# Performance work log

Hardware: AMD Instinct MI355X
Metric: run time of the kernel (lower is better)

Reference implementation:

```python
import jax, jax.numpy as jnp
import numpy as np

N = 50000   # nodes
E = 300000  # directed edges
IN = 512
H = 256
OUT = 256
K = 4096    # K_target; since K < N, pooled node count Kc == K statically


def setup_inputs() -> dict:
    key = jax.random.key(0)
    ks = jax.random.split(key, 8)
    x = jax.random.normal(ks[0], (N, IN), jnp.float32)
    edge_index = jax.random.randint(ks[1], (2, E), 0, N)
    W1 = jax.random.normal(ks[2], (IN, H), jnp.float32) / np.float32(np.sqrt(IN))
    b1 = jnp.zeros((H,), jnp.float32)
    W2 = jax.random.normal(ks[3], (H, OUT), jnp.float32) / np.float32(np.sqrt(H))
    b2 = jnp.zeros((OUT,), jnp.float32)
    w_score = jax.random.normal(ks[4], (H,), jnp.float32) / np.float32(np.sqrt(H))
    W_skip = jax.random.normal(ks[5], (H, OUT), jnp.float32) / np.float32(np.sqrt(H))
    b_skip = jnp.zeros((OUT,), jnp.float32)
    return dict(x=x, edge_index=edge_index, W1=W1, b1=b1, W2=W2, b2=b2,
                w_score=w_score, W_skip=W_skip, b_skip=b_skip)


def _gcn_sparse(x, src, dst, W, b, n):
    # PyG GCNConv(add_self_loops=True, normalize=True): out = D^{-1/2}(A+I)D^{-1/2} x W + b,
    # degrees computed on dst after adding self loops.
    h = x @ W
    loop = jnp.arange(n)
    s = jnp.concatenate([src, loop])
    d = jnp.concatenate([dst, loop])
    deg = jax.ops.segment_sum(jnp.ones_like(d, h.dtype), d, num_segments=n)
    dinv = jnp.where(deg > 0, jax.lax.rsqrt(deg), 0.0)
    coef = (dinv[s] * dinv[d])[:, None]
    return jax.ops.segment_sum(h[s] * coef, d, num_segments=n) + b


def _forward(x, edge_index, W1, b1, W2, b2, w_score, W_skip, b_skip):
    n = x.shape[0]
    src, dst = edge_index[0], edge_index[1]

    # conv1 + relu (dropout is identity in eval mode)
    x1 = jax.nn.relu(_gcn_sparse(x, src, dst, W1, b1, n))
    raw = x1 @ w_score                       # [N] score (Linear, no bias)
    x1g = x1 * jnp.tanh(raw)[:, None]        # gated features

    # top-K node selection
    _, kept = jax.lax.top_k(raw, K)          # sorted descending, like torch.topk
    keep_mask = jnp.zeros((n,), bool).at[kept].set(True)
    deg = jax.ops.segment_sum(jnp.ones((src.shape[0],), jnp.int32), src, num_segments=n)

    # cluster ids: kept nodes get 0..K-1 in topk order
    cid = jnp.full((n,), -1, jnp.int32).at[kept].set(jnp.arange(K, dtype=jnp.int32))

    # non-kept nodes join the kept (undirected) neighbor with max degree;
    # encode (degree, -node_id) so segment_max picks max degree, tie-break smallest id
    s_all = jnp.concatenate([src, dst])
    t_all = jnp.concatenate([dst, src])
    cand = jnp.where(keep_mask[t_all], deg[t_all] * n + (n - 1 - t_all), -1)
    best = jax.ops.segment_max(cand, s_all, num_segments=n)  # empty segs -> int min
    has = best >= 0
    best_t = (n - 1) - jnp.where(has, best % n, 0)
    # global fallback: kept node with max degree (tie-break: earliest in topk order)
    enc_k = deg[kept] * K + (K - 1 - jnp.arange(K))
    bg = kept[jnp.argmax(enc_k)]
    cid = jnp.where(keep_mask, cid, jnp.where(has, cid[best_t], cid[bg]))

    # mean pooling per cluster (pool_by_partition)
    sums = jax.ops.segment_sum(x1g, cid, num_segments=K)
    cnt = jnp.maximum(jax.ops.segment_sum(jnp.ones((n,), x.dtype), cid, num_segments=K), 1.0)
    xp = sums / cnt[:, None]

    # pooled edges with dedup + self-pair removal, as dense KxK adjacency (rows = dst)
    cu, cv = cid[src], cid[dst]
    A = jnp.zeros((K, K), x.dtype).at[cv, cu].max((cu != cv).astype(x.dtype))
    Ahat = A + jnp.eye(K, dtype=x.dtype)
    di = jax.lax.rsqrt(Ahat.sum(axis=1))     # deg >= 1 from self loops
    An = di[:, None] * Ahat * di[None, :]

    # conv2 on pooled graph, broadcast back, skip connection
    xp2 = An @ (xp @ W2) + b2
    return xp2[cid] + x1 @ W_skip + b_skip


def reference(x, edge_index, W1, b1, W2, b2, w_score, W_skip, b_skip):
    return _forward(x, edge_index, W1, b1, W2, b2, w_score, W_skip, b_skip)
```

## Files before the change

### kernel.cpp

```cpp
#include <hip/hip_runtime.h>
#include <hip/hip_bf16.h>

#define N_NODES 50000
#define E_EDGES 300000
#define IN_F 512
#define H_F 256
#define OUT_F 256
#define K_CL 4096
#define KW (K_CL / 32)
#define PCH 128
#define THRESH 192
#define MAXH 1024
#define NSPL 32
#define NB2 ((N_NODES + 255) / 256)
#define KBW ((N_NODES + 63) / 64 + 8)

typedef short bh8 __attribute__((ext_vector_type(8)));
typedef float f4 __attribute__((ext_vector_type(4)));
typedef unsigned short u16;
typedef unsigned long long u64;

__device__ __forceinline__ unsigned fkey(float f) {
    unsigned u = __float_as_uint(f);
    return (u & 0x80000000u) ? ~u : (u | 0x80000000u);
}

__device__ __forceinline__ u16 f2bf(float f) {
    __hip_bfloat16 b = __float2bfloat16(f);
    return *reinterpret_cast<u16*>(&b);
}

__device__ __forceinline__ float bf2f(u16 u) {
    return __uint_as_float(((unsigned)u) << 16);
}

__device__ __forceinline__ int getbit(const u64* __restrict__ bits, int i) {
    return (int)((bits[i >> 6] >> (i & 63)) & 1ULL);
}

__global__ __launch_bounds__(256) void init_nodes(int* cntD, int* degS,
                                                  unsigned long long* best_enc,
                                                  int* bgnode, int* heavycnt,
                                                  unsigned long long* bestpack) {
    int i = blockIdx.x * blockDim.x + threadIdx.x;
    if (i < N_NODES) { cntD[i] = 0; degS[i] = 0; best_enc[i] = 0ULL; }
    if (i == 0) { *heavycnt = 0; *bgnode = 0x7FFFFFFF; *bestpack = 0ULL; }
}

__global__ __launch_bounds__(256) void deg_edges(const int* __restrict__ src,
                                                 const int* __restrict__ dst,
                                                 int* cntD, int* degS) {
    int e = blockIdx.x * blockDim.x + threadIdx.x;
    if (e >= E_EDGES) return;
    atomicAdd(&cntD[dst[e]], 1);
    atomicAdd(&degS[src[e]], 1);
}

#define SBM 64
#define SBN 128
#define SBK 16
__global__ __launch_bounds__(256) void gemm_f32s(const float* __restrict__ A,
                                                 const float* __restrict__ B,
                                                 float* __restrict__ C,
                                                 int M, int Nc, int Kd) {
    __shared__ float As[2][SBM][SBK];
    __shared__ float Bs[2][SBK][SBN];
    int tid = threadIdx.x;
    int tx = tid & 15;
    int ty = tid >> 4;
    int lane = tid & 63;
    int wave = tid >> 6;
    int row0 = blockIdx.y * SBM, col0 = blockIdx.x * SBN;
    float acc[4][8] = {};

    int arow = wave * 16 + (lane >> 2);
    int acolf = ((((lane & 3) * 16) ^ (((lane >> 4) & 1) << 5)) >> 2);

    auto stage_B = [&](int k0, int bb) {
        #pragma unroll
        for (int u = 0; u < 2; ++u) {
            int chunk = wave * 2 + u;
            int krow = chunk * 2 + (lane >> 5);
            const float* gsrc = &B[(long)(k0 + krow) * Nc + col0 + (lane & 31) * 4];
            __builtin_amdgcn_global_load_lds(
                (const __attribute__((address_space(1))) void*)gsrc,
                (__attribute__((address_space(3))) void*)&Bs[bb][chunk * 2][0],
                16, 0, 0);
        }
    };
    auto stage_A = [&](int k0, int bb) {
        int gr = row0 + arow;
        if (gr > M - 1) gr = M - 1;
        const float* gsrc = &A[(long)gr * Kd + k0 + acolf];
        __builtin_amdgcn_global_load_lds(
            (const __attribute__((address_space(1))) void*)gsrc,
            (__attribute__((address_space(3))) void*)&As[bb][wave * 16][0],
            16, 0, 0);
    };
    auto compute = [&](int bb) {
        #pragma unroll
        for (int kq = 0; kq < 4; ++kq) {
            float4 af[4];
            #pragma unroll
            for (int i = 0; i < 4; ++i) {
                int row = ty * 4 + i;
                int cb = ((kq * 16 ^ (((row >> 2) & 1) << 5)) >> 2);
                af[i] = *(const float4*)&As[bb][row][cb];
            }
            #pragma unroll
            for (int kk = 0; kk < 4; ++kk) {
                int k = kq * 4 + kk;
                float4 b0 = *(const float4*)&Bs[bb][k][tx * 4];
                float4 b1 = *(const float4*)&Bs[bb][k][tx * 4 + 64];
                float bv[8] = {b0.x, b0.y, b0.z, b0.w, b1.x, b1.y, b1.z, b1.w};
                float av[4] = {af[0][kk], af[1][kk], af[2][kk], af[3][kk]};
                #pragma unroll
                for (int i = 0; i < 4; ++i)
                    #pragma unroll
                    for (int j = 0; j < 8; ++j)
                        acc[i][j] += av[i] * bv[j];
            }
        }
    };

    stage_B(0, 0);
    stage_A(0, 0);
    __syncthreads();
    int nt = Kd / SBK;
    for (int t = 0; t < nt; ++t) {
        int cb = t & 1;
        if (t + 1 < nt) {
            stage_B(SBK * (t + 1), cb ^ 1);
            stage_A(SBK * (t + 1), cb ^ 1);
        }
        compute(cb);
        __syncthreads();
    }

    #pragma unroll
    for (int i = 0; i < 4; ++i) {
        int gr = row0 + ty * 4 + i;
        if (gr >= M) continue;
        float4 o0 = {acc[i][0], acc[i][1], acc[i][2], acc[i][3]};
        float4 o1 = {acc[i][4], acc[i][5], acc[i][6], acc[i][7]};
        *(float4*)&C[(long)gr * Nc + col0 + tx * 4] = o0;
        *(float4*)&C[(long)gr * Nc + col0 + 64 + tx * 4] = o1;
    }
}

__global__ __launch_bounds__(256) void pack_W2(const float* __restrict__ Wa, u16* Bpa,
                                               const float* __restrict__ Wb, u16* Bpb) {
    int k = blockIdx.x & 255;
    const float* W = (blockIdx.x < 256) ? Wa : Wb;
    u16* Bp = (blockIdx.x < 256) ? Bpa : Bpb;
    int col = threadIdx.x;
    int kb = k >> 5, g = (k >> 3) & 3, j = k & 7;
    Bp[(((long)(kb * 4 + g) * 256) + col) * 8 + j] = f2bf(W[(long)k * 256 + col]);
}

__global__ __launch_bounds__(256) void gemm_mfma(const u16* __restrict__ Ab,
                                                 const float* __restrict__ Af32,
                                                 const int* __restrict__ cnt,
                                                 const u16* __restrict__ Bp,
                                                 float* __restrict__ C,
                                                 int M,
                                                 const int* __restrict__ cid,
                                                 const float* __restrict__ xp2,
                                                 const float* __restrict__ bskip) {
    int tid = threadIdx.x;
    int w = tid >> 6, l = tid & 63;
    int lo16 = l & 15, hi4 = l >> 4;
    int arow = blockIdx.x * 64 + w * 16 + lo16;
    f4 acc[16];
    #pragma unroll
    for (int n = 0; n < 16; ++n) acc[n] = (f4){0.f, 0.f, 0.f, 0.f};

    float s = 1.f;
    if (Af32 && arow < M) s = 1.f / fmaxf((float)cnt[arow], 1.f);

    #pragma unroll
    for (int kb = 0; kb < 8; ++kb) {
        bh8 a = {0, 0, 0, 0, 0, 0, 0, 0};
        if (arow < M) {
            if (Af32) {
                float4 v0 = *(const float4*)&Af32[(long)arow * 256 + kb * 32 + hi4 * 8];
                float4 v1 = *(const float4*)&Af32[(long)arow * 256 + kb * 32 + hi4 * 8 + 4];
                u16 tmp[8] = {f2bf(v0.x * s), f2bf(v0.y * s), f2bf(v0.z * s), f2bf(v0.w * s),
                              f2bf(v1.x * s), f2bf(v1.y * s), f2bf(v1.z * s), f2bf(v1.w * s)};
                a = *(const bh8*)tmp;
            } else {
                a = *(const bh8*)&Ab[(long)arow * 256 + kb * 32 + hi4 * 8];
            }
        }
        const u16* bbase = &Bp[(((long)(kb * 4 + hi4)) * 256 + lo16) * 8];
        #pragma unroll
        for (int n = 0; n < 16; ++n) {
            bh8 b = *(const bh8*)&bbase[(long)n * 128];
            acc[n] = __builtin_amdgcn_mfma_f32_16x16x32_bf16(a, b, acc[n], 0, 0, 0);
        }
    }

    int orow0 = blockIdx.x * 64 + w * 16 + hi4 * 4;
    #pragma unroll
    for (int r = 0; r < 4; ++r) {
        int gr = orow0 + r;
        if (gr >= M) continue;
        long rb = (long)gr * 256;
        const float* xrow = cid ? (xp2 + (long)cid[gr] * 256) : nullptr;
        #pragma unroll
        for (int n = 0; n < 16; ++n) {
            int gc = n * 16 + lo16;
            float v = acc[n][r];
            if (cid) v += xrow[gc] + bskip[gc];
            C[rb + gc] = v;
        }
    }
}

__global__ __launch_bounds__(256) void scan_l1(const int* __restrict__ cnt,
                                               int* bsum, int n, float* dinv) {
    __shared__ int s[256];
    int t = threadIdx.x;
    int i = blockIdx.x * 256 + t;
    int v = (i < n) ? cnt[i] : 0;
    if (dinv && i < n) dinv[i] = rsqrtf((float)v + 1.0f);
    s[t] = v;
    __syncthreads();
    for (int off = 128; off > 0; off >>= 1) {
        if (t < off) s[t] += s[t + off];
        __syncthreads();
    }
    if (t == 0) bsum[blockIdx.x] = s[0];
}

__global__ __launch_bounds__(256) void scan_l2(const int* __restrict__ bsum,
                                               int* bstart, int nb) {
    __shared__ int s[256];
    int t = threadIdx.x;
    int v = (t < nb) ? bsum[t] : 0;
    s[t] = v;
    __syncthreads();
    for (int off = 1; off < 256; off <<= 1) {
        int a = (t >= off) ? s[t - off] : 0;
        __syncthreads();
        s[t] += a;
        __syncthreads();
    }
    if (t < nb) bstart[t] = s[t] - v;
}

__global__ __launch_bounds__(256) void scan_l3(const int* __restrict__ cnt,
                                               const int* __restrict__ bstart,
                                               int* start, int* cur, int n) {
    __shared__ int s[256];
    int t = threadIdx.x;
    int i = blockIdx.x * 256 + t;
    int v = (i < n) ? cnt[i] : 0;
    s[t] = v;
    __syncthreads();
    for (int off = 1; off < 256; off <<= 1) {
        int a = (t >= off) ? s[t - off] : 0;
        __syncthreads();
        s[t] += a;
        __syncthreads();
    }
    int st = bstart[blockIdx.x] + s[t] - v;
    if (i < n) { start[i] = st; cur[i] = st; }
    if (i == n - 1) start[n] = st + v;
}

__global__ __launch_bounds__(256) void csr_scatter(const int* __restrict__ src,
                                                   const int* __restrict__ dst,
                                                   int* cur, int* csr) {
    int e = blockIdx.x * blockDim.x + threadIdx.x;
    if (e >= E_EDGES) return;
    int d = dst[e];
    int p = atomicAdd(&cur[d], 1);
    csr[p] = src[e];
}

__global__ __launch_bounds__(64) void agg_fused(const float* __restrict__ h,
                                                const float* __restrict__ dinv,
                                                const int* __restrict__ rowptr,
                                                const int* __restrict__ csr,
                                                const float* __restrict__ b1,
                                                const float* __restrict__ w_score,
                                                u16* __restrict__ x1b,
                                                float* __restrict__ raw) {
    int i = blockIdx.x;
    int l = threadIdx.x;
    float di_ = dinv[i];
    long hb = (long)i * H_F;
    float sc = di_ * di_;
    float a0 = sc * h[hb + l];
    float a1 = sc * h[hb + l + 64];
    float a2 = sc * h[hb + l + 128];
    float a3 = sc * h[hb + l + 192];
    int p0 = rowptr[i], p1 = rowptr[i + 1];
    for (int t = p0; t < p1; ++t) {
        int s = csr[t];
        float cf = dinv[s] * di_;
        long sb = (long)s * H_F;
        a0 += cf * h[sb + l];
        a1 += cf * h[sb + l + 64];
        a2 += cf * h[sb + l + 128];
        a3 += cf * h[sb + l + 192];
    }
    float v0 = fmaxf(a0 + b1[l], 0.f);
    float v1 = fmaxf(a1 + b1[l + 64], 0.f);
    float v2 = fmaxf(a2 + b1[l + 128], 0.f);
    float v3 = fmaxf(a3 + b1[l + 192], 0.f);
    x1b[hb + l] = f2bf(v0);
    x1b[hb + l + 64] = f2bf(v1);
    x1b[hb + l + 128] = f2bf(v2);
    x1b[hb + l + 192] = f2bf(v3);
    float r0 = v0 * w_score[l];
    float r1 = v1 * w_score[l + 64];
    float r2 = v2 * w_score[l + 128];
    float r3 = v3 * w_score[l + 192];
    float t1 = r0 + r2;
    float t2 = r1 + r3;
    float s2 = t1 + t2;
    #pragma unroll
    for (int off = 32; off > 0; off >>= 1)
        s2 += __shfl_xor(s2, off, 64);
    if (l == 0) raw[i] = s2;
}

__global__ __launch_bounds__(1024) void topk_select(const float* __restrict__ raw,
                                                    unsigned* outT, int* outNeedEq) {
    __shared__ unsigned hist[256];
    __shared__ unsigned sh_prefix;
    __shared__ int sh_k;
    int tid = threadIdx.x;
    if (tid == 0) { sh_prefix = 0; sh_k = K_CL; }
    __syncthreads();
    for (int byte = 3; byte >= 0; --byte) {
        if (tid < 256) hist[tid] = 0;
        __syncthreads();
        unsigned prefix = sh_prefix;
        unsigned known_mask = (byte == 3) ? 0u : (0xFFFFFFFFu << ((byte + 1) * 8));
        for (int i = tid; i < N_NODES; i += 1024) {
            unsigned key = fkey(raw[i]);
            if ((key & known_mask) == prefix)
                atomicAdd(&hist[(key >> (byte * 8)) & 255], 1u);
        }
        __syncthreads();
        if (tid == 0) {
            int kk = sh_k;
            int cum = 0;
            int v = 255;
            for (; v > 0; --v) {
                int c = (int)hist[v];
                if (cum + c >= kk) break;
                cum += c;
            }
            sh_prefix = prefix | ((unsigned)v << (byte * 8));
            sh_k = kk - cum;
        }
        __syncthreads();
    }
    if (tid == 0) { *outT = sh_prefix; *outNeedEq = sh_k; }
}

__global__ __launch_bounds__(256) void topk_count(const float* __restrict__ raw,
                                                  const unsigned* pT,
                                                  int* bGt, int* bEq) {
    __shared__ int sg[256], se[256];
    unsigned T = *pT;
    int t = threadIdx.x;
    int i = blockIdx.x * 256 + t;
    int gt = 0, eq = 0;
    if (i < N_NODES) {
        unsigned k = fkey(raw[i]);
        gt = k > T; eq = (k == T);
    }
    sg[t] = gt; se[t] = eq;
    __syncthreads();
    for (int off = 128; off > 0; off >>= 1) {
        if (t < off) { sg[t] += sg[t + off]; se[t] += se[t + off]; }
        __syncthreads();
    }
    if (t == 0) { bGt[blockIdx.x] = sg[0]; bEq[blockIdx.x] = se[0]; }
}

__global__ __launch_bounds__(256) void scan_blocks(const int* __restrict__ bGt,
                                                   const int* __restrict__ bEq,
                                                   int* gtStart, int* eqStart) {
    __shared__ int sg[256], se[256];
    int t = threadIdx.x;
    int vg = (t < NB2) ? bGt[t] : 0;
    int ve = (t < NB2) ? bEq[t] : 0;
    sg[t] = vg; se[t] = ve;
    __syncthreads();
    for (int off = 1; off < 256; off <<= 1) {
        int a = (t >= off) ? sg[t - off] : 0;
        int b = (t >= off) ? se[t - off] : 0;
        __syncthreads();
        sg[t] += a; se[t] += b;
        __syncthreads();
    }
    if (t < NB2) { gtStart[t] = sg[t] - vg; eqStart[t] = se[t] - ve; }
    if (t == 255) gtStart[NB2] = sg[255];
}

__global__ __launch_bounds__(256) void topk_assign(const float* __restrict__ raw,
                                                   const unsigned* pT, const int* pNeedEq,
                                                   const int* __restrict__ degS,
                                                   const int* __restrict__ gtStart,
                                                   const int* __restrict__ eqStart,
                                                   u64* keep_bits, int* cid,
                                                   unsigned long long* bestpack) {
    __shared__ int sg[256], se[256];
    unsigned T = *pT;
    int needEq = *pNeedEq;
    int totalGt = gtStart[NB2];
    int b = blockIdx.x, t = threadIdx.x;
    int i = b * 256 + t;
    int gt = 0, eq = 0;
    unsigned k = 0;
    if (i < N_NODES) {
        k = fkey(raw[i]);
        gt = k > T; eq = (k == T);
    }
    sg[t] = gt; se[t] = eq;
    __syncthreads();
    for (int off = 1; off < 256; off <<= 1) {
        int a = (t >= off) ? sg[t - off] : 0;
        int c = (t >= off) ? se[t - off] : 0;
        __syncthreads();
        sg[t] += a; se[t] += c;
        __syncthreads();
    }
    int eg = sg[t] - gt, ee = se[t] - eq;
    int kp = 0;
    unsigned long long p = 0ULL;
    if (i < N_NODES) {
        int c = -1;
        if (gt) { kp = 1; c = gtStart[b] + eg; }
        else if (eq) {
            int r = eqStart[b] + ee;
            if (r < needEq) { kp = 1; c = totalGt + r; }
        }
        cid[i] = c;
        if (kp) p = ((unsigned long long)(unsigned)degS[i] << 32) | k;
    }
    u64 ball = __ballot(kp);
    if ((t & 63) == 0) keep_bits[(b * 256 + t) >> 6] = ball;
    #pragma unroll
    for (int o = 32; o > 0; o >>= 1) {
        unsigned long long q = __shfl_xor((long long)p, o, 64);
        if (q > p) p = q;
    }
    if ((t & 63) == 0 && p) atomicMax(bestpack, p);
}

__global__ __launch_bounds__(256) void bg_node(const u64* __restrict__ keep_bits,
                                               const int* __restrict__ degS,
                                               const float* __restrict__ raw,
                                               const unsigned long long* bestpack, int* bgnode) {
    int i = blockIdx.x * blockDim.x + threadIdx.x;
    if (i < N_NODES && getbit(keep_bits, i)) {
        unsigned long long p = ((unsigned long long)(unsigned)degS[i] << 32) | fkey(raw[i]);
        if (p == *bestpack) atomicMin(bgnode, i);
    }
}

__global__ __launch_bounds__(256) void neigh_edges(const int* __restrict__ src,
                                                   const int* __restrict__ dst,
                                                   const u64* __restrict__ keep_bits,
                                                   const int* __restrict__ degS,
                                                   unsigned long long* best_enc) {
    int e = blockIdx.x * blockDim.x + threadIdx.x;
    if (e >= 2 * E_EDGES) return;
    int s, t;
    if (e < E_EDGES) { s = src[e]; t = dst[e]; }
    else { s = dst[e - E_EDGES]; t = src[e - E_EDGES]; }
    if (!getbit(keep_bits, s) && getbit(keep_bits, t)) {
        unsigned long long enc =
            (unsigned long long)((long long)degS[t] * N_NODES + (N_NODES - 1 - t)) + 1ULL;
        atomicMax(&best_enc[s], enc);
    }
}

__global__ __launch_bounds__(256) void resolve_cid(const u64* __restrict__ keep_bits,
                                                   const unsigned long long* __restrict__ best_enc,
                                                   const int* __restrict__ bgnode, int* cid) {
    int i = blockIdx.x * blockDim.x + threadIdx.x;
    if (i >= N_NODES) return;
    if (getbit(keep_bits, i)) return;
    unsigned long long v = best_enc[i];
    if (v > 0ULL) {
        long long enc = (long long)(v - 1ULL);
        int t = (N_NODES - 1) - (int)(enc % N_NODES);
        cid[i] = cid[t];
    } else {
        cid[i] = cid[*bgnode];
    }
}

#define NPB 1024
__global__ __launch_bounds__(256) void ccount2(const int* __restrict__ cid, int* ccnt) {
    __shared__ int hist[K_CL];
    for (int t = threadIdx.x; t < K_CL; t += 256) hist[t] = 0;
    __syncthreads();
    int base = blockIdx.x * NPB;
    #pragma unroll
    for (int u = 0; u < NPB / 256; ++u) {
        int idx = base + u * 256 + threadIdx.x;
        if (idx < N_NODES) atomicAdd(&hist[cid[idx]], 1);
    }
    __syncthreads();
    for (int t = threadIdx.x; t < K_CL; t += 256) {
        int hh = hist[t];
        if (hh) atomicAdd(&ccnt[t], hh);
    }
}

__global__ __launch_bounds__(256) void cscatter2(const int* __restrict__ cid,
                                                 int* ccur, int* clist) {
    __shared__ int hist[K_CL];
    for (int t = threadIdx.x; t < K_CL; t += 256) hist[t] = 0;
    __syncthreads();
    int base = blockIdx.x * NPB;
    int myc[NPB / 256], myr[NPB / 256];
    #pragma unroll
    for (int u = 0; u < NPB / 256; ++u) {
        int idx = base + u * 256 + threadIdx.x;
        if (idx < N_NODES) { myc[u] = cid[idx]; myr[u] = atomicAdd(&hist[myc[u]], 1); }
        else myc[u] = -1;
    }
    __syncthreads();
    for (int t = threadIdx.x; t < K_CL; t += 256) {
        int hh = hist[t];
        if (hh) hist[t] = atomicAdd(&ccur[t], hh);
    }
    __syncthreads();
    #pragma unroll
    for (int u = 0; u < NPB / 256; ++u)
        if (myc[u] >= 0) clist[hist[myc[u]] + myr[u]] = base + u * 256 + threadIdx.x;
}

__global__ __launch_bounds__(256) void pool_chunk(const u16* __restrict__ x1b,
                                                  const float* __restrict__ raw,
                                                  const int* __restrict__ clist,
                                                  const int* __restrict__ cid,
                                                  float* xp) {
    __shared__ int s_node[PCH];
    __shared__ int s_c[PCH];
    __shared__ float s_g[PCH];
    int j = threadIdx.x;
    int base = blockIdx.x * PCH;
    int m = N_NODES - base; if (m > PCH) m = PCH;
    for (int t = j; t < m; t += 256) {
        int nd = clist[base + t];
        s_node[t] = nd;
        s_c[t] = cid[nd];
        s_g[t] = tanhf(raw[nd]);
    }
    __syncthreads();
    float acc = 0.f;
    int cprev = s_c[0];
    for (int t = 0; t < m; t += 4) {
        int mm = m - t; if (mm > 4) mm = 4;
        float v[4];
        #pragma unroll
        for (int u = 0; u < 4; ++u)
            if (u < mm) v[u] = bf2f(x1b[(long)s_node[t + u] * H_F + j]);
        #pragma unroll
        for (int u = 0; u < 4; ++u) {
            if (u < mm) {
                int c = s_c[t + u];
                if (c != cprev) {
                    atomicAdd(&xp[(long)cprev * H_F + j], acc);
                    acc = 0.f;
                    cprev = c;
                }
                acc += s_g[t + u] * v[u];
            }
        }
    }
    atomicAdd(&xp[(long)cprev * H_F + j], acc);
}

__global__ __launch_bounds__(256) void build_Abits(const int* __restrict__ src,
                                                   const int* __restrict__ dst,
                                                   const int* __restrict__ cid,
                                                   unsigned* Abits) {
    int e = blockIdx.x * blockDim.x + threadIdx.x;
    if (e >= E_EDGES) return;
    int cu = cid[src[e]], cv = cid[dst[e]];
    if (cu != cv) atomicOr(&Abits[(long)cv * KW + (cu >> 5)], 1u << (cu & 31));
}

__global__ __launch_bounds__(256) void pop_di2(const unsigned* __restrict__ Abits, float* di,
                                               int* nnzA, int* heavy, int* heavycnt) {
    int i = blockIdx.x * blockDim.x + threadIdx.x;
    if (i >= K_CL) return;
    int c = 0;
    for (int w = 0; w < KW; ++w) c += __popc(Abits[(long)i * KW + w]);
    di[i] = rsqrtf((float)c + 1.0f);
    nnzA[i] = c;
    if (c > THRESH) {
        int p = atomicAdd(heavycnt, 1);
        if (p < MAXH) heavy[p] = i;
    }
}

__global__ __launch_bounds__(256) void spmm_light(const unsigned* __restrict__ Abits,
                                                  const float* __restrict__ xpW2,
                                                  const float* __restrict__ di,
                                                  const float* __restrict__ b2,
                                                  const int* __restrict__ nnzA,
                                                  float* xp2) {
    __shared__ unsigned s_row[KW];
    __shared__ float s_part[3][256];
    int cv = blockIdx.x;
    if (nnzA[cv] > THRESH) return;
    int tid = threadIdx.x;
    int w = tid >> 6, l = tid & 63;
    if (tid < KW) s_row[tid] = Abits[(long)cv * KW + tid];
    __syncthreads();
    float4 a0 = {0.f, 0.f, 0.f, 0.f}, a1 = {0.f, 0.f, 0.f, 0.f};
    const float4* Y4 = (const float4*)xpW2;
    for (int wi = w * 32; wi < w * 32 + 32; wi += 2) {
        unsigned w0 = s_row[wi], w1 = s_row[wi + 1];
        while (w0 | w1) {
            if (w0) {
                int b = __ffs(w0) - 1; w0 &= w0 - 1;
                int cu = wi * 32 + b;
                float d = di[cu];
                float4 y = Y4[(long)cu * 64 + l];
                a0.x += d * y.x; a0.y += d * y.y; a0.z += d * y.z; a0.w += d * y.w;
            }
            if (w1) {
                int b = __ffs(w1) - 1; w1 &= w1 - 1;
                int cu = (wi + 1) * 32 + b;
                float d = di[cu];
                float4 y = Y4[(long)cu * 64 + l];
                a1.x += d * y.x; a1.y += d * y.y; a1.z += d * y.z; a1.w += d * y.w;
            }
        }
    }
    float4 acc = {a0.x + a1.x, a0.y + a1.y, a0.z + a1.z, a0.w + a1.w};
    if (w > 0) *(float4*)&s_part[w - 1][l * 4] = acc;
    __syncthreads();
    if (w == 0) {
        #pragma unroll
        for (int ww = 0; ww < 3; ++ww) {
            float4 p = *(float4*)&s_part[ww][l * 4];
            acc.x += p.x; acc.y += p.y; acc.z += p.z; acc.w += p.w;
        }
        float dv = di[cv];
        float4 ys = Y4[(long)cv * 64 + l];
        float4 o;
        o.x = dv * (acc.x + dv * ys.x) + b2[l * 4 + 0];
        o.y = dv * (acc.y + dv * ys.y) + b2[l * 4 + 1];
        o.z = dv * (acc.z + dv * ys.z) + b2[l * 4 + 2];
        o.w = dv * (acc.w + dv * ys.w) + b2[l * 4 + 3];
        *(float4*)&xp2[(long)cv * H_F + l * 4] = o;
    }
}

__global__ __launch_bounds__(256) void spmm_heavy(const unsigned* __restrict__ Abits,
                                                  const float* __restrict__ xpW2,
                                                  const float* __restrict__ di,
                                                  const int* __restrict__ heavy,
                                                  const int* __restrict__ heavycnt,
                                                  float* Zacc) {
    __shared__ float s_part[3][256];
    int hi = blockIdx.x;
    int cnt = *heavycnt; if (cnt > MAXH) cnt = MAXH;
    if (hi >= cnt) return;
    int cv = heavy[hi];
    int sp = blockIdx.y;
    int tid = threadIdx.x;
    int w = tid >> 6, l = tid & 63;
    int wi = sp * (KW / NSPL) + w;
    unsigned word = Abits[(long)cv * KW + wi];
    float4 acc = {0.f, 0.f, 0.f, 0.f};
    const float4* Y4 = (const float4*)xpW2;
    while (word) {
        int b = __ffs(word) - 1; word &= word - 1;
        int cu = wi * 32 + b;
        float d = di[cu];
        float4 y = Y4[(long)cu * 64 + l];
        acc.x += d * y.x; acc.y += d * y.y; acc.z += d * y.z; acc.w += d * y.w;
    }
    if (w > 0) *(float4*)&s_part[w - 1][l * 4] = acc;
    __syncthreads();
    if (w == 0) {
        #pragma unroll
        for (int ww = 0; ww < 3; ++ww) {
            float4 p = *(float4*)&s_part[ww][l * 4];
            acc.x += p.x; acc.y += p.y; acc.z += p.z; acc.w += p.w;
        }
        float* zp = &Zacc[(long)cv * H_F + l * 4];
        atomicAdd(zp + 0, acc.x);
        atomicAdd(zp + 1, acc.y);
        atomicAdd(zp + 2, acc.z);
        atomicAdd(zp + 3, acc.w);
    }
}

__global__ __launch_bounds__(256) void heavy_epi(const float* __restrict__ Zacc,
                                                 const float* __restrict__ xpW2,
                                                 const float* __restrict__ di,
                                                 const float* __restrict__ b2,
                                                 const int* __restrict__ heavy,
                                                 const int* __restrict__ heavycnt,
                                                 float* xp2) {
    int hi = blockIdx.x;
    int cnt = *heavycnt; if (cnt > MAXH) cnt = MAXH;
    if (hi >= cnt) return;
    int cv = heavy[hi];
    int j = threadIdx.x;
    float dv = di[cv];
    xp2[(long)cv * H_F + j] =
        dv * (Zacc[(long)cv * H_F + j] + dv * xpW2[(long)cv * H_F + j]) + b2[j];
}

static inline size_t align256(size_t x) { return (x + 255) & ~(size_t)255; }

extern "C" void kernel_launch(void* const* d_in, const int* in_sizes, int n_in,
                              void* d_out, int out_size, void* d_ws, size_t ws_size,
                              hipStream_t stream) {
    const float* x      = (const float*)d_in[0];
    const int*   eidx   = (const int*)d_in[1];
    const float* W1     = (const float*)d_in[2];
    const float* b1     = (const float*)d_in[3];
    const float* W2     = (const float*)d_in[4];
    const float* b2     = (const float*)d_in[5];
    const float* wscore = (const float*)d_in[6];
    const float* Wskip  = (const float*)d_in[7];
    const float* bskip  = (const float*)d_in[8];
    float* out = (float*)d_out;

    const int* src = eidx;
    const int* dst = eidx + E_EDGES;

    char* ws = (char*)d_ws;
    size_t off = 0;
    auto alloc = [&](size_t bytes) { char* p = ws + off; off += align256(bytes); return p; };

    float* h     = (float*)alloc((size_t)N_NODES * H_F * 4);
    u16*   x1b   = (u16*)alloc((size_t)N_NODES * H_F * 2);
    float* raw   = (float*)alloc((size_t)N_NODES * 4);
    float* dinv  = (float*)alloc((size_t)N_NODES * 4);
    int*   cntD  = (int*)alloc((size_t)N_NODES * 4);
    int*   degS  = (int*)alloc((size_t)N_NODES * 4);
    u64*   keep_bits = (u64*)alloc((size_t)KBW * 8);
    int*   cid   = (int*)alloc((size_t)N_NODES * 4);
    unsigned long long* best_enc = (unsigned long long*)alloc((size_t)N_NODES * 8);
    int*   rowptr= (int*)alloc((size_t)(N_NODES + 1) * 4);
    int*   cur   = (int*)alloc((size_t)N_NODES * 4);
    int*   csr   = (int*)alloc((size_t)E_EDGES * 4);
    int*   ccnt  = (int*)alloc((size_t)K_CL * 4);
    int*   cstart= (int*)alloc((size_t)(K_CL + 1) * 4);
    int*   ccur  = (int*)alloc((size_t)K_CL * 4);
    int*   clist = (int*)alloc((size_t)N_NODES * 4);
    int*   bGt   = (int*)alloc((size_t)NB2 * 4);
    int*   bEq   = (int*)alloc((size_t)NB2 * 4);
    int*   gtStart = (int*)alloc((size_t)(NB2 + 1) * 4);
    int*   eqStart = (int*)alloc((size_t)NB2 * 4);
    int*   bsum  = (int*)alloc((size_t)256 * 4);
    int*   bstart= (int*)alloc((size_t)256 * 4);
    char*  small = alloc(64);
    unsigned* selT = (unsigned*)(small + 0);
    int* needEq    = (int*)(small + 4);
    int* bgnode    = (int*)(small + 8);
    int* heavycnt  = (int*)(small + 12);
    unsigned long long* bestpack = (unsigned long long*)(small + 16);
    float* xp    = (float*)alloc((size_t)K_CL * H_F * 4);
    unsigned* Abits = (unsigned*)alloc((size_t)K_CL * KW * 4);
    float* Zacc  = (float*)alloc((size_t)K_CL * H_F * 4);
    float* di    = (float*)alloc((size_t)K_CL * 4);
    int*   nnzA  = (int*)alloc((size_t)K_CL * 4);
    int*   heavy = (int*)alloc((size_t)MAXH * 4);
    float* xpW2  = (float*)alloc((size_t)K_CL * H_F * 4);
    float* xp2   = (float*)alloc((size_t)K_CL * H_F * 4);
    u16*  BpS   = (u16*)alloc((size_t)H_F * OUT_F * 2);
    u16*  Bp2   = (u16*)alloc((size_t)H_F * H_F * 2);
    (void)ws_size; (void)n_in; (void)in_sizes; (void)out_size;

    int nb = NB2;
    int eb = (E_EDGES + 255) / 256;

    init_nodes<<<nb, 256, 0, stream>>>(cntD, degS, best_enc, bgnode, heavycnt, bestpack);
    deg_edges<<<eb, 256, 0, stream>>>(src, dst, cntD, degS);

    pack_W2<<<512, 256, 0, stream>>>(Wskip, BpS, W2, Bp2);

    {
        dim3 grid(H_F / SBN, (N_NODES + SBM - 1) / SBM);
        gemm_f32s<<<grid, 256, 0, stream>>>(x, W1, h, N_NODES, H_F, IN_F);
    }

    scan_l1<<<NB2, 256, 0, stream>>>(cntD, bsum, N_NODES, dinv);
    scan_l2<<<1, 256, 0, stream>>>(bsum, bstart, NB2);
    scan_l3<<<NB2, 256, 0, stream>>>(cntD, bstart, rowptr, cur, N_NODES);
    csr_scatter<<<eb, 256, 0, stream>>>(src, dst, cur, csr);
    agg_fused<<<N_NODES, 64, 0, stream>>>(h, dinv, rowptr, csr, b1, wscore, x1b, raw);

    topk_select<<<1, 1024, 0, stream>>>(raw, selT, needEq);
    topk_count<<<NB2, 256, 0, stream>>>(raw, selT, bGt, bEq);
    scan_blocks<<<1, 256, 0, stream>>>(bGt, bEq, gtStart, eqStart);
    topk_assign<<<NB2, 256, 0, stream>>>(raw, selT, needEq, degS, gtStart, eqStart,
                                         keep_bits, cid, bestpack);
    bg_node<<<nb, 256, 0, stream>>>(keep_bits, degS, raw, bestpack, bgnode);

    neigh_edges<<<(2 * E_EDGES + 255) / 256, 256, 0, stream>>>(src, dst, keep_bits, degS,
                                                               best_enc);
    resolve_cid<<<nb, 256, 0, stream>>>(keep_bits, best_enc, bgnode, cid);

    hipMemsetAsync(xp, 0, (size_t)K_CL * H_F * 4 * 2 + (size_t)K_CL * KW * 4, stream);

    hipMemsetAsync(ccnt, 0, (size_t)K_CL * 4, stream);
    {
        int cb = (N_NODES + NPB - 1) / NPB;
        ccount2<<<cb, 256, 0, stream>>>(cid, ccnt);
        scan_l1<<<K_CL / 256, 256, 0, stream>>>(ccnt, bsum, K_CL, nullptr);
        scan_l2<<<1, 256, 0, stream>>>(bsum, bstart, K_CL / 256);
        scan_l3<<<K_CL / 256, 256, 0, stream>>>(ccnt, bstart, cstart, ccur, K_CL);
        cscatter2<<<cb, 256, 0, stream>>>(cid, ccur, clist);
    }
    pool_chunk<<<(N_NODES + PCH - 1) / PCH, 256, 0, stream>>>(x1b, raw, clist, cid, xp);

    gemm_mfma<<<K_CL / 64, 256, 0, stream>>>(nullptr, xp, ccnt, Bp2, xpW2, K_CL,
                                             nullptr, nullptr, nullptr);

    build_Abits<<<eb, 256, 0, stream>>>(src, dst, cid, Abits);
    pop_di2<<<(K_CL + 255) / 256, 256, 0, stream>>>(Abits, di, nnzA, heavy, heavycnt);
    spmm_light<<<K_CL, 256, 0, stream>>>(Abits, xpW2, di, b2, nnzA, xp2);
    {
        dim3 hgrid(MAXH, NSPL);
        spmm_heavy<<<hgrid, 256, 0, stream>>>(Abits, xpW2, di, heavy, heavycnt, Zacc);
    }
    heavy_epi<<<MAXH, 256, 0, stream>>>(Zacc, xpW2, di, b2, heavy, heavycnt, xp2);

    gemm_mfma<<<(N_NODES + 63) / 64, 256, 0, stream>>>(x1b, nullptr, nullptr, BpS, out,
                                                       N_NODES, cid, xp2, bskip);
}
```

Measured before the change: 680.6 us.

## Parallelize top-k radix select across many blocks with per-byte histogram kernels

Replaces the single-block 1024-thread radix select over 50000 scores with four rounds of a grid-wide histogram kernel followed by a one-thread pick kernel. The prefix and remaining count now live in global memory and are initialized in init_nodes, and the per-byte histograms are zeroed by a memset. The goal is to remove the serial single-CU pass over all nodes. The cost is eight extra small kernel launches plus global atomics.

Result: faster. 659.5 us (-3.1%).

```diff
diff --git a/kernel.cpp b/kernel.cpp
--- a/kernel.cpp
+++ b/kernel.cpp
@@ -41,10 +41,14 @@
 __global__ __launch_bounds__(256) void init_nodes(int* cntD, int* degS,
                                                   unsigned long long* best_enc,
                                                   int* bgnode, int* heavycnt,
-                                                  unsigned long long* bestpack) {
+                                                  unsigned long long* bestpack,
+                                                  unsigned* selT, int* curk) {
     int i = blockIdx.x * blockDim.x + threadIdx.x;
     if (i < N_NODES) { cntD[i] = 0; degS[i] = 0; best_enc[i] = 0ULL; }
-    if (i == 0) { *heavycnt = 0; *bgnode = 0x7FFFFFFF; *bestpack = 0ULL; }
+    if (i == 0) {
+        *heavycnt = 0; *bgnode = 0x7FFFFFFF; *bestpack = 0ULL;
+        *selT = 0u; *curk = K_CL;
+    }
 }
 
 __global__ __launch_bounds__(256) void deg_edges(const int* __restrict__ src,
@@ -327,40 +331,38 @@
     if (l == 0) raw[i] = s2;
 }
 
-__global__ __launch_bounds__(1024) void topk_select(const float* __restrict__ raw,
-                                                    unsigned* outT, int* outNeedEq) {
-    __shared__ unsigned hist[256];
-    __shared__ unsigned sh_prefix;
-    __shared__ int sh_k;
-    int tid = threadIdx.x;
-    if (tid == 0) { sh_prefix = 0; sh_k = K_CL; }
-    __syncthreads();
-    for (int byte = 3; byte >= 0; --byte) {
-        if (tid < 256) hist[tid] = 0;
-        __syncthreads();
-        unsigned prefix = sh_prefix;
+__global__ __launch_bounds__(256) void radix_hist(const float* __restrict__ raw,
+                                                  const unsigned* __restrict__ pPrefix,
+                                                  int byte, int* hist) {
+    __shared__ int lh[256];
+    int t = threadIdx.x;
+    lh[t] = 0;
+    __syncthreads();
+    int i = blockIdx.x * 256 + t;
+    if (i < N_NODES) {
+        unsigned key = fkey(raw[i]);
         unsigned known_mask = (byte == 3) ? 0u : (0xFFFFFFFFu << ((byte + 1) * 8));
-        for (int i = tid; i < N_NODES; i += 1024) {
-            unsigned key = fkey(raw[i]);
-            if ((key & known_mask) == prefix)
-                atomicAdd(&hist[(key >> (byte * 8)) & 255], 1u);
-        }
-        __syncthreads();
-        if (tid == 0) {
-            int kk = sh_k;
-            int cum = 0;
-            int v = 255;
-            for (; v > 0; --v) {
-                int c = (int)hist[v];
-                if (cum + c >= kk) break;
-                cum += c;
-            }
-            sh_prefix = prefix | ((unsigned)v << (byte * 8));
-            sh_k = kk - cum;
-        }
-        __syncthreads();
-    }
-    if (tid == 0) { *outT = sh_prefix; *outNeedEq = sh_k; }
+        if ((key & known_mask) == *pPrefix)
+            atomicAdd(&lh[(key >> (byte * 8)) & 255], 1);
+    }
+    __syncthreads();
+    int hh = lh[t];
+    if (hh) atomicAdd(&hist[t], hh);
+}
+
+__global__ __launch_bounds__(64) void radix_pick(const int* __restrict__ hist,
+                                                 unsigned* pPrefix, int* pK, int byte) {
+    if (threadIdx.x != 0) return;
+    int kk = *pK;
+    int cum = 0;
+    int v = 255;
+    for (; v > 0; --v) {
+        int c = hist[v];
+        if (cum + c >= kk) break;
+        cum += c;
+    }
+    *pPrefix |= ((unsigned)v) << (byte * 8);
+    *pK = kk - cum;
 }
 
 __global__ __launch_bounds__(256) void topk_count(const float* __restrict__ raw,
@@ -765,6 +767,7 @@
     int*   eqStart = (int*)alloc((size_t)NB2 * 4);
     int*   bsum  = (int*)alloc((size_t)256 * 4);
     int*   bstart= (int*)alloc((size_t)256 * 4);
+    int*   hist4 = (int*)alloc((size_t)4 * 256 * 4);
     char*  small = alloc(64);
     unsigned* selT = (unsigned*)(small + 0);
     int* needEq    = (int*)(small + 4);
@@ -786,8 +789,10 @@
     int nb = NB2;
     int eb = (E_EDGES + 255) / 256;
 
-    init_nodes<<<nb, 256, 0, stream>>>(cntD, degS, best_enc, bgnode, heavycnt, bestpack);
+    init_nodes<<<nb, 256, 0, stream>>>(cntD, degS, best_enc, bgnode, heavycnt, bestpack,
+                                       selT, needEq);
     deg_edges<<<eb, 256, 0, stream>>>(src, dst, cntD, degS);
+    hipMemsetAsync(hist4, 0, 4 * 256 * 4, stream);
 
     pack_W2<<<512, 256, 0, stream>>>(Wskip, BpS, W2, Bp2);
 
@@ -802,7 +807,10 @@
     csr_scatter<<<eb, 256, 0, stream>>>(src, dst, cur, csr);
     agg_fused<<<N_NODES, 64, 0, stream>>>(h, dinv, rowptr, csr, b1, wscore, x1b, raw);
 
-    topk_select<<<1, 1024, 0, stream>>>(raw, selT, needEq);
+    for (int b = 3; b >= 0; --b) {
+        radix_hist<<<NB2, 256, 0, stream>>>(raw, selT, b, hist4 + b * 256);
+        radix_pick<<<1, 64, 0, stream>>>(hist4 + b * 256, selT, needEq, b);
+    }
     topk_count<<<NB2, 256, 0, stream>>>(raw, selT, bGt, bEq);
     scan_blocks<<<1, 256, 0, stream>>>(bGt, bEq, gtStart, eqStart);
     topk_assign<<<NB2, 256, 0, stream>>>(raw, selT, needEq, degS, gtStart, eqStart,
```
